# Kernel optimization log

Hardware: AMD Instinct MI355X
Metric: run time of the kernel (lower is better)

The kernel has to match this reference:

```python
import jax, jax.numpy as jnp
import numpy as np

RES = 300
NC = 48
N_PTS = 1_000_000


def _bilinear2d(params, gx, gy):
    """params: (C,R,R); gx,gy: (N,) in [-1,1]. grid_sample align_corners=True,
    gx indexes width (last axis), gy indexes height."""
    C, R, _ = params.shape
    px = (gx + 1.0) * 0.5 * (R - 1)
    py = (gy + 1.0) * 0.5 * (R - 1)
    x0f = jnp.floor(px)
    y0f = jnp.floor(py)
    wx = px - x0f
    wy = py - y0f
    x0 = jnp.clip(x0f.astype(jnp.int32), 0, R - 1)
    x1 = jnp.clip(x0 + 1, 0, R - 1)
    y0 = jnp.clip(y0f.astype(jnp.int32), 0, R - 1)
    y1 = jnp.clip(y0 + 1, 0, R - 1)
    f00 = params[:, y0, x0]  # (C,N)
    f01 = params[:, y0, x1]
    f10 = params[:, y1, x0]
    f11 = params[:, y1, x1]
    return (f00 * (1 - wx) * (1 - wy) + f01 * wx * (1 - wy)
            + f10 * (1 - wx) * wy + f11 * wx * wy)


def _linear1d(params, gy):
    """params: (C,R) (line grid with width 1, x-coord fixed at 0); gy: (N,)."""
    C, R = params.shape
    py = (gy + 1.0) * 0.5 * (R - 1)
    y0f = jnp.floor(py)
    wy = py - y0f
    y0 = jnp.clip(y0f.astype(jnp.int32), 0, R - 1)
    y1 = jnp.clip(y0 + 1, 0, R - 1)
    return params[:, y0] * (1 - wy) + params[:, y1] * wy  # (C,N)


def setup_inputs() -> dict:
    key = jax.random.key(0)
    k1, k2, k3 = jax.random.split(key, 3)
    x = jax.random.uniform(k1, (N_PTS, 3), dtype=jnp.float32)
    plane_params = 0.1 * jax.random.normal(k2, (3, NC, RES, RES), dtype=jnp.float32)
    line_params = 0.1 * jax.random.normal(k3, (3, NC, RES, 1), dtype=jnp.float32)
    return {"x": x, "plane_params": plane_params, "line_params": line_params}


def reference(x, plane_params, line_params):
    N = x.shape[0]
    xs = 2.0 * x - 1.0  # (N,3)
    # grid_sample grid is (x_coord, y_coord): plane pairs [0,1],[0,2],[1,2]
    gx = jnp.stack([xs[:, 0], xs[:, 0], xs[:, 1]])  # (3,N) width coord
    gy = jnp.stack([xs[:, 1], xs[:, 2], xs[:, 2]])  # (3,N) height coord
    gl = jnp.stack([xs[:, 2], xs[:, 1], xs[:, 0]])  # (3,N) line coord
    plane_f = jax.vmap(_bilinear2d)(plane_params, gx, gy)      # (3,C,N)
    line_f = jax.vmap(_linear1d)(line_params[..., 0], gl)      # (3,C,N)
    feats = (plane_f * line_f).reshape(3 * NC, N).T            # (N, 3C)
    return feats
```

## Files before the change

### kernel.cpp

```cpp
#include <hip/hip_runtime.h>
#include <hip/hip_fp16.h>

#define RES 300
#define NC 48
#define RES2 (RES * RES)
#define CELLS 64
#define NBINS (CELLS*CELLS*CELLS)
#define SCAN_T 1024
#define SCAN_BLK (NBINS / SCAN_T)
#define TPP 12

typedef float f32x4 __attribute__((ext_vector_type(4)));
typedef unsigned int u32x4 __attribute__((ext_vector_type(4)));

struct alignas(8) h4 { __half2 h[2]; };

__device__ __forceinline__ int clampi(int v, int lo, int hi) {
    return v < lo ? lo : (v > hi ? hi : v);
}

__device__ __forceinline__ unsigned spread3(unsigned v) {
    v = (v | (v << 16)) & 0x030000FFu;
    v = (v | (v << 8))  & 0x0300F00Fu;
    v = (v | (v << 4))  & 0x030C30C3u;
    v = (v | (v << 2))  & 0x09249249u;
    return v;
}

__device__ __forceinline__ unsigned morton_key(float a, float b, float c) {
    unsigned ca = (unsigned)clampi((int)(a * (float)CELLS), 0, CELLS - 1);
    unsigned cb = (unsigned)clampi((int)(b * (float)CELLS), 0, CELLS - 1);
    unsigned cc = (unsigned)clampi((int)(c * (float)CELLS), 0, CELLS - 1);
    return spread3(ca) | (spread3(cb) << 1) | (spread3(cc) << 2);
}


__global__ __launch_bounds__(256) void tp_tables_kernel(const float* __restrict__ pin,
                                                        const float* __restrict__ lin,
                                                        __half* __restrict__ pout,
                                                        __half* __restrict__ lout) {
    unsigned idx = blockIdx.x * 256u + threadIdx.x;
    if (idx < 3u * RES2) {
        unsigned p  = idx / RES2;
        unsigned yx = idx - p * RES2;
        const float* src = pin + (size_t)p * NC * RES2 + yx;
        unsigned short v[NC];
#pragma unroll
        for (int c = 0; c < NC; ++c) {
            __half h = __float2half(src[(size_t)c * RES2]);
            v[c] = *reinterpret_cast<unsigned short*>(&h);
        }
        u32x4* dst = reinterpret_cast<u32x4*>(pout + (size_t)idx * NC);
#pragma unroll
        for (int i = 0; i < 6; ++i) {
            u32x4 w;
            w.x = (unsigned)v[8 * i + 0] | ((unsigned)v[8 * i + 1] << 16);
            w.y = (unsigned)v[8 * i + 2] | ((unsigned)v[8 * i + 3] << 16);
            w.z = (unsigned)v[8 * i + 4] | ((unsigned)v[8 * i + 5] << 16);
            w.w = (unsigned)v[8 * i + 6] | ((unsigned)v[8 * i + 7] << 16);
            dst[i] = w;
        }
    } else {
        unsigned li = idx - 3u * RES2;
        if (li >= 3u * RES) return;
        unsigned p = li / RES;
        unsigned y = li - p * RES;
#pragma unroll
        for (int c = 0; c < NC; ++c)
            lout[(size_t)li * NC + c] = __float2half(lin[((size_t)p * NC + c) * RES + y]);
    }
}


__global__ __launch_bounds__(256) void zero_bins_kernel(unsigned* __restrict__ counts) {
    unsigned i = blockIdx.x * 256u + threadIdx.x;
    if (i < NBINS) counts[i] = 0u;
}

__global__ __launch_bounds__(256) void hist_kernel(const float* __restrict__ x,
                                                   unsigned* __restrict__ counts,
                                                   unsigned N) {
    unsigned i = blockIdx.x * 256u + threadIdx.x;
    if (i >= N) return;
    unsigned k = morton_key(x[3u * i], x[3u * i + 1u], x[3u * i + 2u]);
    atomicAdd(&counts[k], 1u);
}

__global__ __launch_bounds__(SCAN_T) void scan1_kernel(const unsigned* __restrict__ counts,
                                                       unsigned* __restrict__ pre,
                                                       unsigned* __restrict__ bsum) {
    __shared__ unsigned part[SCAN_T];
    unsigned b = blockIdx.x * SCAN_T + threadIdx.x;
    int t = threadIdx.x;
    unsigned c = counts[b];
    part[t] = c;
    __syncthreads();
    for (int d = 1; d < SCAN_T; d <<= 1) {
        unsigned v = (t >= d) ? part[t - d] : 0u;
        __syncthreads();
        part[t] += v;
        __syncthreads();
    }
    pre[b] = part[t] - c;
    if (t == SCAN_T - 1) bsum[blockIdx.x] = part[t];
}

__global__ __launch_bounds__(SCAN_BLK) void scan2_kernel(unsigned* __restrict__ bsum,
                                                         unsigned* __restrict__ boff) {
    __shared__ unsigned part[SCAN_BLK];
    int t = threadIdx.x;
    unsigned c = bsum[t];
    part[t] = c;
    __syncthreads();
    for (int d = 1; d < SCAN_BLK; d <<= 1) {
        unsigned v = (t >= d) ? part[t - d] : 0u;
        __syncthreads();
        part[t] += v;
        __syncthreads();
    }
    boff[t] = part[t] - c;
}

__global__ __launch_bounds__(SCAN_T) void scan3_kernel(const unsigned* __restrict__ pre,
                                                       const unsigned* __restrict__ boff,
                                                       unsigned* __restrict__ offs) {
    unsigned b = blockIdx.x * SCAN_T + threadIdx.x;
    offs[b] = pre[b] + boff[blockIdx.x];
}

__global__ __launch_bounds__(256) void scatter_kernel(const float* __restrict__ x,
                                                      unsigned* __restrict__ offs,
                                                      f32x4* __restrict__ sorted,
                                                      unsigned N) {
    unsigned i = blockIdx.x * 256u + threadIdx.x;
    if (i >= N) return;
    float a = x[3u * i], b = x[3u * i + 1u], c = x[3u * i + 2u];
    unsigned k = morton_key(a, b, c);
    unsigned pos = atomicAdd(&offs[k], 1u);
    f32x4 v;
    v.x = a; v.y = b; v.z = c; v.w = __uint_as_float(i);
    sorted[pos] = v;
}


__global__ __launch_bounds__(256) void encode_sorted_kernel(const f32x4* __restrict__ sorted,
                                                            const __half* __restrict__ pt,
                                                            const __half* __restrict__ lt,
                                                            float* __restrict__ out,
                                                            unsigned N) {
    unsigned nwg  = gridDim.x;
    unsigned orig = blockIdx.x;
    unsigned xcd = orig & 7u, j = orig >> 3u;
    unsigned qq = nwg >> 3u, r = nwg & 7u;
    unsigned bid = (xcd < r ? xcd * (qq + 1u) : r * (qq + 1u) + (xcd - r) * qq) + j;

    unsigned gid = bid * 256u + threadIdx.x;
    if (gid >= N * TPP) return;
    unsigned s  = gid / TPP;
    unsigned c4 = gid - s * TPP;

    f32x4 pv4 = sorted[s];
    unsigned n = __float_as_uint(pv4.w);
    float xs0 = pv4.x, xs1 = pv4.y, xs2 = pv4.z;

    unsigned cbase = c4 * 4u;

    h4 c00_0, c01_0, c10_0, c11_0, L0_0, L1_0;
    h4 c00_1, c01_1, c10_1, c11_1, L0_1, L1_1;
    h4 c00_2, c01_2, c10_2, c11_2, L0_2, L1_2;
    float w00_[3], w01_[3], w10_[3], w11_[3], wl_[3];

#pragma unroll
    for (int p = 0; p < 3; ++p) {
        float gxv = (p == 2) ? xs1 : xs0;
        float gyv = (p == 0) ? xs1 : xs2;
        float glv = (p == 0) ? xs2 : ((p == 1) ? xs1 : xs0);

        float gxs = 2.0f * gxv - 1.0f;
        float gys = 2.0f * gyv - 1.0f;
        float gls = 2.0f * glv - 1.0f;
        float px = (gxs + 1.0f) * 0.5f * (float)(RES - 1);
        float py = (gys + 1.0f) * 0.5f * (float)(RES - 1);
        float pl = (gls + 1.0f) * 0.5f * (float)(RES - 1);

        float x0f = floorf(px), y0f = floorf(py), l0f = floorf(pl);
        float wx = px - x0f, wy = py - y0f, wl = pl - l0f;

        int ix0 = clampi((int)x0f, 0, RES - 1);
        int ix1 = ix0 + 1 > RES - 1 ? RES - 1 : ix0 + 1;
        int iy0 = clampi((int)y0f, 0, RES - 1);
        int iy1 = iy0 + 1 > RES - 1 ? RES - 1 : iy0 + 1;
        int il0 = clampi((int)l0f, 0, RES - 1);
        int il1 = il0 + 1 > RES - 1 ? RES - 1 : il0 + 1;

        w00_[p] = (1.0f - wx) * (1.0f - wy);
        w01_[p] = wx * (1.0f - wy);
        w10_[p] = (1.0f - wx) * wy;
        w11_[p] = wx * wy;
        wl_[p]  = wl;

        const __half* pb = pt + (size_t)p * RES2 * NC;
        const __half* lb = lt + (size_t)p * RES * NC + cbase;
        unsigned o00 = ((unsigned)iy0 * RES + (unsigned)ix0) * NC + cbase;
        unsigned o01 = ((unsigned)iy0 * RES + (unsigned)ix1) * NC + cbase;
        unsigned o10 = ((unsigned)iy1 * RES + (unsigned)ix0) * NC + cbase;
        unsigned o11 = ((unsigned)iy1 * RES + (unsigned)ix1) * NC + cbase;

        h4 a = *reinterpret_cast<const h4*>(pb + o00);
        h4 b = *reinterpret_cast<const h4*>(pb + o01);
        h4 c = *reinterpret_cast<const h4*>(pb + o10);
        h4 d = *reinterpret_cast<const h4*>(pb + o11);
        h4 e = *reinterpret_cast<const h4*>(lb + (size_t)il0 * NC);
        h4 f = *reinterpret_cast<const h4*>(lb + (size_t)il1 * NC);
        if (p == 0) { c00_0 = a; c01_0 = b; c10_0 = c; c11_0 = d; L0_0 = e; L1_0 = f; }
        if (p == 1) { c00_1 = a; c01_1 = b; c10_1 = c; c11_1 = d; L0_1 = e; L1_1 = f; }
        if (p == 2) { c00_2 = a; c01_2 = b; c10_2 = c; c11_2 = d; L0_2 = e; L1_2 = f; }
    }

    float* ob = out + (size_t)n * 144u + cbase;

#pragma unroll
    for (int p = 0; p < 3; ++p) {
        h4 v00 = (p == 0) ? c00_0 : (p == 1) ? c00_1 : c00_2;
        h4 v01 = (p == 0) ? c01_0 : (p == 1) ? c01_1 : c01_2;
        h4 v10 = (p == 0) ? c10_0 : (p == 1) ? c10_1 : c10_2;
        h4 v11 = (p == 0) ? c11_0 : (p == 1) ? c11_1 : c11_2;
        h4 vl0 = (p == 0) ? L0_0  : (p == 1) ? L0_1  : L0_2;
        h4 vl1 = (p == 0) ? L1_0  : (p == 1) ? L1_1  : L1_2;

        float2 f00a = __half22float2(v00.h[0]), f00b = __half22float2(v00.h[1]);
        float2 f01a = __half22float2(v01.h[0]), f01b = __half22float2(v01.h[1]);
        float2 f10a = __half22float2(v10.h[0]), f10b = __half22float2(v10.h[1]);
        float2 f11a = __half22float2(v11.h[0]), f11b = __half22float2(v11.h[1]);
        float2 l0a  = __half22float2(vl0.h[0]), l0b  = __half22float2(vl0.h[1]);
        float2 l1a  = __half22float2(vl1.h[0]), l1b  = __half22float2(vl1.h[1]);

        float w00 = w00_[p], w01 = w01_[p], w10 = w10_[p], w11 = w11_[p];
        float wl = wl_[p], wl0 = 1.0f - wl;

        f32x4 plane_v;
        plane_v.x = f00a.x * w00 + f01a.x * w01 + f10a.x * w10 + f11a.x * w11;
        plane_v.y = f00a.y * w00 + f01a.y * w01 + f10a.y * w10 + f11a.y * w11;
        plane_v.z = f00b.x * w00 + f01b.x * w01 + f10b.x * w10 + f11b.x * w11;
        plane_v.w = f00b.y * w00 + f01b.y * w01 + f10b.y * w10 + f11b.y * w11;

        f32x4 line_v;
        line_v.x = l0a.x * wl0 + l1a.x * wl;
        line_v.y = l0a.y * wl0 + l1a.y * wl;
        line_v.z = l0b.x * wl0 + l1b.x * wl;
        line_v.w = l0b.y * wl0 + l1b.y * wl;

        f32x4 rr = plane_v * line_v;
        __builtin_nontemporal_store(rr, reinterpret_cast<f32x4*>(ob + p * 48));
    }
}


__global__ __launch_bounds__(256) void encode_kernel(const float* __restrict__ x,
                                                     const __half* __restrict__ pt,
                                                     const __half* __restrict__ lt,
                                                     float* __restrict__ out,
                                                     unsigned N) {
    unsigned gid = blockIdx.x * 256u + threadIdx.x;
    if (gid >= N * 36u) return;
    unsigned n  = gid / 36u;
    unsigned q  = gid - n * 36u;
    unsigned p  = q / 12u;
    unsigned c4 = q - p * 12u;

    float xv0 = x[3u * n + 0u];
    float xv1 = x[3u * n + 1u];
    float xv2 = x[3u * n + 2u];
    float gxv = (p == 2u) ? xv1 : xv0;
    float gyv = (p == 0u) ? xv1 : xv2;
    float glv = (p == 0u) ? xv2 : ((p == 1u) ? xv1 : xv0);

    float gxs = 2.0f * gxv - 1.0f;
    float gys = 2.0f * gyv - 1.0f;
    float gls = 2.0f * glv - 1.0f;
    float px = (gxs + 1.0f) * 0.5f * (float)(RES - 1);
    float py = (gys + 1.0f) * 0.5f * (float)(RES - 1);
    float pl = (gls + 1.0f) * 0.5f * (float)(RES - 1);

    float x0f = floorf(px), y0f = floorf(py), l0f = floorf(pl);
    float wx = px - x0f, wy = py - y0f, wl = pl - l0f;

    int ix0 = clampi((int)x0f, 0, RES - 1);
    int ix1 = ix0 + 1 > RES - 1 ? RES - 1 : ix0 + 1;
    int iy0 = clampi((int)y0f, 0, RES - 1);
    int iy1 = iy0 + 1 > RES - 1 ? RES - 1 : iy0 + 1;
    int il0 = clampi((int)l0f, 0, RES - 1);
    int il1 = il0 + 1 > RES - 1 ? RES - 1 : il0 + 1;

    unsigned cbase = c4 * 4u;
    const __half* pb = pt + (size_t)p * RES2 * NC;
    h4 v00 = *reinterpret_cast<const h4*>(pb + ((unsigned)iy0 * RES + (unsigned)ix0) * NC + cbase);
    h4 v01 = *reinterpret_cast<const h4*>(pb + ((unsigned)iy0 * RES + (unsigned)ix1) * NC + cbase);
    h4 v10 = *reinterpret_cast<const h4*>(pb + ((unsigned)iy1 * RES + (unsigned)ix0) * NC + cbase);
    h4 v11 = *reinterpret_cast<const h4*>(pb + ((unsigned)iy1 * RES + (unsigned)ix1) * NC + cbase);

    float2 f00a = __half22float2(v00.h[0]), f00b = __half22float2(v00.h[1]);
    float2 f01a = __half22float2(v01.h[0]), f01b = __half22float2(v01.h[1]);
    float2 f10a = __half22float2(v10.h[0]), f10b = __half22float2(v10.h[1]);
    float2 f11a = __half22float2(v11.h[0]), f11b = __half22float2(v11.h[1]);

    float w00 = (1.0f - wx) * (1.0f - wy);
    float w01 = wx * (1.0f - wy);
    float w10 = (1.0f - wx) * wy;
    float w11 = wx * wy;

    f32x4 plane_v;
    plane_v.x = f00a.x * w00 + f01a.x * w01 + f10a.x * w10 + f11a.x * w11;
    plane_v.y = f00a.y * w00 + f01a.y * w01 + f10a.y * w10 + f11a.y * w11;
    plane_v.z = f00b.x * w00 + f01b.x * w01 + f10b.x * w10 + f11b.x * w11;
    plane_v.w = f00b.y * w00 + f01b.y * w01 + f10b.y * w10 + f11b.y * w11;

    const __half* lb = lt + (size_t)p * RES * NC + cbase;
    h4 vl0 = *reinterpret_cast<const h4*>(lb + (size_t)il0 * NC);
    h4 vl1 = *reinterpret_cast<const h4*>(lb + (size_t)il1 * NC);
    float2 l0a = __half22float2(vl0.h[0]), l0b = __half22float2(vl0.h[1]);
    float2 l1a = __half22float2(vl1.h[0]), l1b = __half22float2(vl1.h[1]);

    float wl0 = 1.0f - wl;
    f32x4 line_v;
    line_v.x = l0a.x * wl0 + l1a.x * wl;
    line_v.y = l0a.y * wl0 + l1a.y * wl;
    line_v.z = l0b.x * wl0 + l1b.x * wl;
    line_v.w = l0b.y * wl0 + l1b.y * wl;

    f32x4 rr = plane_v * line_v;
    __builtin_nontemporal_store(rr, reinterpret_cast<f32x4*>(out + (size_t)n * 144u + (size_t)q * 4u));
}

__global__ __launch_bounds__(256) void encode_fallback_kernel(const float* __restrict__ x,
                                                              const float* __restrict__ plane,
                                                              const float* __restrict__ line,
                                                              float* __restrict__ out,
                                                              unsigned N) {
    unsigned gid = blockIdx.x * 256u + threadIdx.x;
    if (gid >= N * 36u) return;
    unsigned n  = gid / 36u;
    unsigned q  = gid - n * 36u;
    unsigned p  = q / 12u;
    unsigned c4 = q - p * 12u;

    float xv0 = x[3u * n + 0u];
    float xv1 = x[3u * n + 1u];
    float xv2 = x[3u * n + 2u];
    float gxv = (p == 2u) ? xv1 : xv0;
    float gyv = (p == 0u) ? xv1 : xv2;
    float glv = (p == 0u) ? xv2 : ((p == 1u) ? xv1 : xv0);

    float gxs = 2.0f * gxv - 1.0f;
    float gys = 2.0f * gyv - 1.0f;
    float gls = 2.0f * glv - 1.0f;
    float px = (gxs + 1.0f) * 0.5f * (float)(RES - 1);
    float py = (gys + 1.0f) * 0.5f * (float)(RES - 1);
    float pl = (gls + 1.0f) * 0.5f * (float)(RES - 1);

    float x0f = floorf(px), y0f = floorf(py), l0f = floorf(pl);
    float wx = px - x0f, wy = py - y0f, wl = pl - l0f;

    int ix0 = clampi((int)x0f, 0, RES - 1);
    int ix1 = ix0 + 1 > RES - 1 ? RES - 1 : ix0 + 1;
    int iy0 = clampi((int)y0f, 0, RES - 1);
    int iy1 = iy0 + 1 > RES - 1 ? RES - 1 : iy0 + 1;
    int il0 = clampi((int)l0f, 0, RES - 1);
    int il1 = il0 + 1 > RES - 1 ? RES - 1 : il0 + 1;

    float w00 = (1.0f - wx) * (1.0f - wy);
    float w01 = wx * (1.0f - wy);
    float w10 = (1.0f - wx) * wy;
    float w11 = wx * wy;
    float wl0 = 1.0f - wl;

    float4 r;
    float* rp = &r.x;
#pragma unroll
    for (int cc = 0; cc < 4; ++cc) {
        unsigned c = c4 * 4u + (unsigned)cc;
        const float* pp = plane + ((size_t)p * NC + c) * RES2;
        float f00 = pp[(size_t)iy0 * RES + ix0];
        float f01 = pp[(size_t)iy0 * RES + ix1];
        float f10 = pp[(size_t)iy1 * RES + ix0];
        float f11 = pp[(size_t)iy1 * RES + ix1];
        float pv = f00 * w00 + f01 * w01 + f10 * w10 + f11 * w11;
        const float* lp = line + ((size_t)p * NC + c) * RES;
        float lv = lp[il0] * wl0 + lp[il1] * wl;
        rp[cc] = pv * lv;
    }
    *reinterpret_cast<float4*>(out + (size_t)n * 144u + (size_t)q * 4u) = r;
}

extern "C" void kernel_launch(void* const* d_in, const int* in_sizes, int n_in,
                              void* d_out, int out_size, void* d_ws, size_t ws_size,
                              hipStream_t stream) {
    const float* x     = (const float*)d_in[0];
    const float* plane = (const float*)d_in[1];
    const float* line  = (const float*)d_in[2];
    float* out = (float*)d_out;
    unsigned N = (unsigned)(in_sizes[0] / 3);

    size_t plane_t_elems = (size_t)3 * RES2 * NC;
    size_t line_t_elems  = (size_t)3 * RES * NC;
    size_t sorted_bytes  = (size_t)N * 16u;
    size_t plane_bytes   = plane_t_elems * sizeof(__half);
    size_t line_bytes    = line_t_elems * sizeof(__half);
    size_t bins_bytes    = (size_t)NBINS * 4u;
    size_t bsum_bytes    = (size_t)SCAN_BLK * 4u;

    size_t need_mid  = plane_bytes + line_bytes;
    size_t need_full = sorted_bytes + plane_bytes + line_bytes + 3u * bins_bytes + 2u * bsum_bytes;

    unsigned pblocks = (N + 255u) / 256u;
    unsigned tpblocks = (3u * RES2 + 3u * RES + 255u) / 256u;

    if (ws_size >= need_full) {
        char* base = (char*)d_ws;
        f32x4*   sorted  = (f32x4*)base;    base += sorted_bytes;
        __half*  plane_t = (__half*)base;   base += plane_bytes;
        __half*  line_t  = (__half*)base;   base += line_bytes;
        unsigned* counts = (unsigned*)base; base += bins_bytes;
        unsigned* pre    = (unsigned*)base; base += bins_bytes;
        unsigned* offs   = (unsigned*)base; base += bins_bytes;
        unsigned* bsum   = (unsigned*)base; base += bsum_bytes;
        unsigned* boff   = (unsigned*)base;

        unsigned total  = N * TPP;
        unsigned blocks = (total + 255u) / 256u;

        zero_bins_kernel<<<(NBINS + 255) / 256, 256, 0, stream>>>(counts);
        hist_kernel<<<pblocks, 256, 0, stream>>>(x, counts, N);
        tp_tables_kernel<<<tpblocks, 256, 0, stream>>>(plane, line, plane_t, line_t);
        scan1_kernel<<<SCAN_BLK, SCAN_T, 0, stream>>>(counts, pre, bsum);
        scan2_kernel<<<1, SCAN_BLK, 0, stream>>>(bsum, boff);
        scan3_kernel<<<SCAN_BLK, SCAN_T, 0, stream>>>(pre, boff, offs);
        scatter_kernel<<<pblocks, 256, 0, stream>>>(x, offs, sorted, N);
        encode_sorted_kernel<<<blocks, 256, 0, stream>>>(sorted, plane_t, line_t, out, N);
    } else if (ws_size >= need_mid) {
        __half* plane_t = (__half*)d_ws;
        __half* line_t  = plane_t + plane_t_elems;
        unsigned total  = N * 36u;
        unsigned blocks = (total + 255u) / 256u;
        tp_tables_kernel<<<tpblocks, 256, 0, stream>>>(plane, line, plane_t, line_t);
        encode_kernel<<<blocks, 256, 0, stream>>>(x, plane_t, line_t, out, N);
    } else {
        unsigned total  = N * 36u;
        unsigned blocks = (total + 255u) / 256u;
        encode_fallback_kernel<<<blocks, 256, 0, stream>>>(x, plane, line, out, N);
    }
}
```

Measured before the change: 273.9 us.

## Stage encoded features in shared memory for coalesced output stores, widen gathers

Each block of 192 threads now handles 32 sorted points, six threads per point with 8 channels each, so table gathers use 16-byte loads. Results go to a padded LDS buffer and are then written out cooperatively as contiguous 576-byte rows per original point. Previously each thread wrote scattered 16-byte pieces. This aims to make the scattered writes to the 576 MB output more coalesced, and halves the thread count per point. The cost is a __syncthreads, LDS traffic and lower per-block parallelism.

```diff
diff --git a/kernel.cpp b/kernel.cpp
--- a/kernel.cpp
+++ b/kernel.cpp
@@ -8,12 +8,15 @@
 #define NBINS (CELLS*CELLS*CELLS)
 #define SCAN_T 1024
 #define SCAN_BLK (NBINS / SCAN_T)
-#define TPP 12
+#define PPB 32
+#define EBLK 192
+#define ROWC 37
 
 typedef float f32x4 __attribute__((ext_vector_type(4)));
 typedef unsigned int u32x4 __attribute__((ext_vector_type(4)));
 
-struct alignas(8) h4 { __half2 h[2]; };
+struct alignas(8)  h4 { __half2 h[2]; };
+struct alignas(16) h8 { __half2 h[4]; };
 
 __device__ __forceinline__ int clampi(int v, int lo, int hi) {
     return v < lo ? lo : (v > hi ? hi : v);
@@ -143,115 +146,116 @@
 }
 
 
-__global__ __launch_bounds__(256) void encode_sorted_kernel(const f32x4* __restrict__ sorted,
-                                                            const __half* __restrict__ pt,
-                                                            const __half* __restrict__ lt,
-                                                            float* __restrict__ out,
-                                                            unsigned N) {
+__global__ __launch_bounds__(EBLK) void encode_sorted_kernel(const f32x4* __restrict__ sorted,
+                                                             const __half* __restrict__ pt,
+                                                             const __half* __restrict__ lt,
+                                                             float* __restrict__ out,
+                                                             unsigned N) {
     unsigned nwg  = gridDim.x;
     unsigned orig = blockIdx.x;
-    unsigned xcd = orig & 7u, j = orig >> 3u;
-    unsigned qq = nwg >> 3u, r = nwg & 7u;
-    unsigned bid = (xcd < r ? xcd * (qq + 1u) : r * (qq + 1u) + (xcd - r) * qq) + j;
-
-    unsigned gid = bid * 256u + threadIdx.x;
-    if (gid >= N * TPP) return;
-    unsigned s  = gid / TPP;
-    unsigned c4 = gid - s * TPP;
-
-    f32x4 pv4 = sorted[s];
-    unsigned n = __float_as_uint(pv4.w);
-    float xs0 = pv4.x, xs1 = pv4.y, xs2 = pv4.z;
-
-    unsigned cbase = c4 * 4u;
-
-    h4 c00_0, c01_0, c10_0, c11_0, L0_0, L1_0;
-    h4 c00_1, c01_1, c10_1, c11_1, L0_1, L1_1;
-    h4 c00_2, c01_2, c10_2, c11_2, L0_2, L1_2;
-    float w00_[3], w01_[3], w10_[3], w11_[3], wl_[3];
-
-#pragma unroll
-    for (int p = 0; p < 3; ++p) {
-        float gxv = (p == 2) ? xs1 : xs0;
-        float gyv = (p == 0) ? xs1 : xs2;
-        float glv = (p == 0) ? xs2 : ((p == 1) ? xs1 : xs0);
-
-        float gxs = 2.0f * gxv - 1.0f;
-        float gys = 2.0f * gyv - 1.0f;
-        float gls = 2.0f * glv - 1.0f;
-        float px = (gxs + 1.0f) * 0.5f * (float)(RES - 1);
-        float py = (gys + 1.0f) * 0.5f * (float)(RES - 1);
-        float pl = (gls + 1.0f) * 0.5f * (float)(RES - 1);
-
-        float x0f = floorf(px), y0f = floorf(py), l0f = floorf(pl);
-        float wx = px - x0f, wy = py - y0f, wl = pl - l0f;
-
-        int ix0 = clampi((int)x0f, 0, RES - 1);
-        int ix1 = ix0 + 1 > RES - 1 ? RES - 1 : ix0 + 1;
-        int iy0 = clampi((int)y0f, 0, RES - 1);
-        int iy1 = iy0 + 1 > RES - 1 ? RES - 1 : iy0 + 1;
-        int il0 = clampi((int)l0f, 0, RES - 1);
-        int il1 = il0 + 1 > RES - 1 ? RES - 1 : il0 + 1;
-
-        w00_[p] = (1.0f - wx) * (1.0f - wy);
-        w01_[p] = wx * (1.0f - wy);
-        w10_[p] = (1.0f - wx) * wy;
-        w11_[p] = wx * wy;
-        wl_[p]  = wl;
-
-        const __half* pb = pt + (size_t)p * RES2 * NC;
-        const __half* lb = lt + (size_t)p * RES * NC + cbase;
-        unsigned o00 = ((unsigned)iy0 * RES + (unsigned)ix0) * NC + cbase;
-        unsigned o01 = ((unsigned)iy0 * RES + (unsigned)ix1) * NC + cbase;
-        unsigned o10 = ((unsigned)iy1 * RES + (unsigned)ix0) * NC + cbase;
-        unsigned o11 = ((unsigned)iy1 * RES + (unsigned)ix1) * NC + cbase;
-
-        h4 a = *reinterpret_cast<const h4*>(pb + o00);
-        h4 b = *reinterpret_cast<const h4*>(pb + o01);
-        h4 c = *reinterpret_cast<const h4*>(pb + o10);
-        h4 d = *reinterpret_cast<const h4*>(pb + o11);
-        h4 e = *reinterpret_cast<const h4*>(lb + (size_t)il0 * NC);
-        h4 f = *reinterpret_cast<const h4*>(lb + (size_t)il1 * NC);
-        if (p == 0) { c00_0 = a; c01_0 = b; c10_0 = c; c11_0 = d; L0_0 = e; L1_0 = f; }
-        if (p == 1) { c00_1 = a; c01_1 = b; c10_1 = c; c11_1 = d; L0_1 = e; L1_1 = f; }
-        if (p == 2) { c00_2 = a; c01_2 = b; c10_2 = c; c11_2 = d; L0_2 = e; L1_2 = f; }
-    }
-
-    float* ob = out + (size_t)n * 144u + cbase;
-
-#pragma unroll
-    for (int p = 0; p < 3; ++p) {
-        h4 v00 = (p == 0) ? c00_0 : (p == 1) ? c00_1 : c00_2;
-        h4 v01 = (p == 0) ? c01_0 : (p == 1) ? c01_1 : c01_2;
-        h4 v10 = (p == 0) ? c10_0 : (p == 1) ? c10_1 : c10_2;
-        h4 v11 = (p == 0) ? c11_0 : (p == 1) ? c11_1 : c11_2;
-        h4 vl0 = (p == 0) ? L0_0  : (p == 1) ? L0_1  : L0_2;
-        h4 vl1 = (p == 0) ? L1_0  : (p == 1) ? L1_1  : L1_2;
-
-        float2 f00a = __half22float2(v00.h[0]), f00b = __half22float2(v00.h[1]);
-        float2 f01a = __half22float2(v01.h[0]), f01b = __half22float2(v01.h[1]);
-        float2 f10a = __half22float2(v10.h[0]), f10b = __half22float2(v10.h[1]);
-        float2 f11a = __half22float2(v11.h[0]), f11b = __half22float2(v11.h[1]);
-        float2 l0a  = __half22float2(vl0.h[0]), l0b  = __half22float2(vl0.h[1]);
-        float2 l1a  = __half22float2(vl1.h[0]), l1b  = __half22float2(vl1.h[1]);
-
-        float w00 = w00_[p], w01 = w01_[p], w10 = w10_[p], w11 = w11_[p];
-        float wl = wl_[p], wl0 = 1.0f - wl;
-
-        f32x4 plane_v;
-        plane_v.x = f00a.x * w00 + f01a.x * w01 + f10a.x * w10 + f11a.x * w11;
-        plane_v.y = f00a.y * w00 + f01a.y * w01 + f10a.y * w10 + f11a.y * w11;
-        plane_v.z = f00b.x * w00 + f01b.x * w01 + f10b.x * w10 + f11b.x * w11;
-        plane_v.w = f00b.y * w00 + f01b.y * w01 + f10b.y * w10 + f11b.y * w11;
-
-        f32x4 line_v;
-        line_v.x = l0a.x * wl0 + l1a.x * wl;
-        line_v.y = l0a.y * wl0 + l1a.y * wl;
-        line_v.z = l0b.x * wl0 + l1b.x * wl;
-        line_v.w = l0b.y * wl0 + l1b.y * wl;
-
-        f32x4 rr = plane_v * line_v;
-        __builtin_nontemporal_store(rr, reinterpret_cast<f32x4*>(ob + p * 48));
+    unsigned xcd = orig & 7u, j0 = orig >> 3u;
+    unsigned qq = nwg >> 3u, rr = nwg & 7u;
+    unsigned bid = (xcd < rr ? xcd * (qq + 1u) : rr * (qq + 1u) + (xcd - rr) * qq) + j0;
+
+    __shared__ f32x4 fbuf[PPB * ROWC];
+    __shared__ unsigned nbuf[PPB];
+
+    unsigned t   = threadIdx.x;
+    unsigned ptl = t / 6u;
+    unsigned c8  = t - ptl * 6u;
+    unsigned B0  = bid * PPB;
+    unsigned s   = B0 + ptl;
+
+    if (s < N) {
+        f32x4 pv4 = sorted[s];
+        unsigned n = __float_as_uint(pv4.w);
+        if (c8 == 0u) nbuf[ptl] = n;
+        float xs0 = pv4.x, xs1 = pv4.y, xs2 = pv4.z;
+        unsigned cb = c8 * 8u;
+
+#pragma unroll
+        for (int p = 0; p < 3; ++p) {
+            float gxv = (p == 2) ? xs1 : xs0;
+            float gyv = (p == 0) ? xs1 : xs2;
+            float glv = (p == 0) ? xs2 : ((p == 1) ? xs1 : xs0);
+
+            float gxs = 2.0f * gxv - 1.0f;
+            float gys = 2.0f * gyv - 1.0f;
+            float gls = 2.0f * glv - 1.0f;
+            float px = (gxs + 1.0f) * 0.5f * (float)(RES - 1);
+            float py = (gys + 1.0f) * 0.5f * (float)(RES - 1);
+            float pl = (gls + 1.0f) * 0.5f * (float)(RES - 1);
+
+            float x0f = floorf(px), y0f = floorf(py), l0f = floorf(pl);
+            float wx = px - x0f, wy = py - y0f, wl = pl - l0f;
+
+            int ix0 = clampi((int)x0f, 0, RES - 1);
+            int ix1 = ix0 + 1 > RES - 1 ? RES - 1 : ix0 + 1;
+            int iy0 = clampi((int)y0f, 0, RES - 1);
+            int iy1 = iy0 + 1 > RES - 1 ? RES - 1 : iy0 + 1;
+            int il0 = clampi((int)l0f, 0, RES - 1);
+            int il1 = il0 + 1 > RES - 1 ? RES - 1 : il0 + 1;
+
+            const __half* pb = pt + (size_t)p * RES2 * NC;
+            const __half* lb = lt + (size_t)p * RES * NC + cb;
+            unsigned o00 = ((unsigned)iy0 * RES + (unsigned)ix0) * NC + cb;
+            unsigned o01 = ((unsigned)iy0 * RES + (unsigned)ix1) * NC + cb;
+            unsigned o10 = ((unsigned)iy1 * RES + (unsigned)ix0) * NC + cb;
+            unsigned o11 = ((unsigned)iy1 * RES + (unsigned)ix1) * NC + cb;
+
+            h8 v00 = *reinterpret_cast<const h8*>(pb + o00);
+            h8 v01 = *reinterpret_cast<const h8*>(pb + o01);
+            h8 v10 = *reinterpret_cast<const h8*>(pb + o10);
+            h8 v11 = *reinterpret_cast<const h8*>(pb + o11);
+            h8 vl0 = *reinterpret_cast<const h8*>(lb + (size_t)il0 * NC);
+            h8 vl1 = *reinterpret_cast<const h8*>(lb + (size_t)il1 * NC);
+
+            float w00 = (1.0f - wx) * (1.0f - wy);
+            float w01 = wx * (1.0f - wy);
+            float w10 = (1.0f - wx) * wy;
+            float w11 = wx * wy;
+            float wl0 = 1.0f - wl;
+
+            f32x4 r0, r1;
+#pragma unroll
+            for (int jj = 0; jj < 4; ++jj) {
+                float2 a00 = __half22float2(v00.h[jj]);
+                float2 a01 = __half22float2(v01.h[jj]);
+                float2 a10 = __half22float2(v10.h[jj]);
+                float2 a11 = __half22float2(v11.h[jj]);
+                float2 b0  = __half22float2(vl0.h[jj]);
+                float2 b1  = __half22float2(vl1.h[jj]);
+                float pvx = a00.x * w00 + a01.x * w01 + a10.x * w10 + a11.x * w11;
+                float pvy = a00.y * w00 + a01.y * w01 + a10.y * w10 + a11.y * w11;
+                float lvx = b0.x * wl0 + b1.x * wl;
+                float lvy = b0.y * wl0 + b1.y * wl;
+                float rx = pvx * lvx;
+                float ry = pvy * lvy;
+                if (jj == 0) { r0.x = rx; r0.y = ry; }
+                if (jj == 1) { r0.z = rx; r0.w = ry; }
+                if (jj == 2) { r1.x = rx; r1.y = ry; }
+                if (jj == 3) { r1.z = rx; r1.w = ry; }
+            }
+
+            f32x4* dst = &fbuf[ptl * ROWC + (unsigned)p * 12u + c8 * 2u];
+            dst[0] = r0;
+            dst[1] = r1;
+        }
+    }
+    __syncthreads();
+
+    unsigned rem = N - B0;
+    unsigned vp = rem < PPB ? rem : PPB;
+    unsigned nchunk = vp * 36u;
+#pragma unroll
+    for (int j = 0; j < 6; ++j) {
+        unsigned c = (unsigned)j * EBLK + t;
+        if (c < nchunk) {
+            unsigned row = c / 36u;
+            unsigned off = c - row * 36u;
+            f32x4 v = fbuf[row * ROWC + off];
+            __builtin_nontemporal_store(v, reinterpret_cast<f32x4*>(out + (size_t)nbuf[row] * 144u + off * 4u));
+        }
     }
 }
 
@@ -412,7 +416,7 @@
     size_t need_mid  = plane_bytes + line_bytes;
     size_t need_full = sorted_bytes + plane_bytes + line_bytes + 3u * bins_bytes + 2u * bsum_bytes;
 
-    unsigned pblocks = (N + 255u) / 256u;
+    unsigned pblocks  = (N + 255u) / 256u;
     unsigned tpblocks = (3u * RES2 + 3u * RES + 255u) / 256u;
 
     if (ws_size >= need_full) {
@@ -426,8 +430,7 @@
         unsigned* bsum   = (unsigned*)base; base += bsum_bytes;
         unsigned* boff   = (unsigned*)base;
 
-        unsigned total  = N * TPP;
-        unsigned blocks = (total + 255u) / 256u;
+        unsigned eblocks = (N + PPB - 1u) / PPB;
 
         zero_bins_kernel<<<(NBINS + 255) / 256, 256, 0, stream>>>(counts);
         hist_kernel<<<pblocks, 256, 0, stream>>>(x, counts, N);
@@ -436,7 +439,7 @@
         scan2_kernel<<<1, SCAN_BLK, 0, stream>>>(bsum, boff);
         scan3_kernel<<<SCAN_BLK, SCAN_T, 0, stream>>>(pre, boff, offs);
         scatter_kernel<<<pblocks, 256, 0, stream>>>(x, offs, sorted, N);
-        encode_sorted_kernel<<<blocks, 256, 0, stream>>>(sorted, plane_t, line_t, out, N);
+        encode_sorted_kernel<<<eblocks, EBLK, 0, stream>>>(sorted, plane_t, line_t, out, N);
     } else if (ws_size >= need_mid) {
         __half* plane_t = (__half*)d_ws;
         __half* line_t  = plane_t + plane_t_elems;
```

Measured after the change: 263.5 us. 1.04x faster.
